# Performance work log

Hardware: AMD Instinct MI355X
Metric: run time of the kernel (lower is better)

## Reference

```python
import jax, jax.numpy as jnp
import numpy as np

B, T, V, E, H = 256, 512, 50000, 300, 128
NORM_GAIN = 0.8     # norm_gain fed at train time
FORGET_BIAS = 1.0
EPS = 1e-12         # tf.contrib.layers.layer_norm default epsilon


def setup_inputs() -> dict:
    key = jax.random.key(0)
    k1, k2, k3 = jax.random.split(key, 3)
    x = jax.random.randint(k1, (B, T), 0, V, dtype=jnp.int32)
    embed = jax.random.normal(k2, (V, E), dtype=jnp.float32)  # tf.random_normal stddev=1
    W = jax.random.normal(k3, (E + H, 4 * H), dtype=jnp.float32) / np.float32(np.sqrt(E + H))
    gains = jnp.full((5, H), NORM_GAIN, dtype=jnp.float32)   # i, j, f, o, cell-transform
    shifts = jnp.zeros((5, H), dtype=jnp.float32)
    return {"x": x, "embed": embed, "W": W, "gains": gains, "shifts": shifts}


def _ln(v, g, b):
    # layer norm over feature axis with learned gain/shift
    m = jnp.mean(v, axis=-1, keepdims=True)
    var = jnp.mean(jnp.square(v - m), axis=-1, keepdims=True)
    return (v - m) * jax.lax.rsqrt(var + EPS) * g + b


def reference(x, embed, W, gains, shifts):
    # embedding: einsum('abc,cd->abd', one_hot(x), embed) == embed[x]
    xe = jnp.take(embed, x, axis=0)            # [B, T, E]
    xe = jnp.transpose(xe, (1, 0, 2))          # [T, B, E] for scan
    c0 = jnp.zeros((x.shape[0], H), jnp.float32)
    h0 = c0

    def step(carry, x_t):
        c, h = carry
        z = jnp.concatenate([x_t, h], axis=-1) @ W      # [B, 4H], no bias
        i, j, f, o = jnp.split(z, 4, axis=-1)
        i = _ln(i, gains[0], shifts[0])
        j = _ln(j, gains[1], shifts[1])
        f = _ln(f, gains[2], shifts[2])
        o = _ln(o, gains[3], shifts[3])
        g = jax.nn.relu(j)                              # activation=tf.nn.relu
        new_c = c * jax.nn.sigmoid(f + FORGET_BIAS) + jax.nn.sigmoid(i) * g
        new_h = jax.nn.relu(_ln(new_c, gains[4], shifts[4])) * jax.nn.sigmoid(o)
        return (new_c, new_h), new_h

    _, ys = jax.lax.scan(step, (c0, h0), xe)            # ys: [T, B, H]
    return jnp.transpose(ys, (1, 0, 2))                 # [B, T, H]
```

## Files before the change

### kernel.cpp

```cpp
#include <hip/hip_runtime.h>
#include <math.h>

#define Bb   256
#define Tt   512
#define Vv   50000
#define Ee   300
#define Hh   128
#define G4   512
#define EPS  1e-12f
#define FBIAS 1.0f
#define RPB  4
#define NBLK (Bb / RPB)

typedef _Float16 half8 __attribute__((ext_vector_type(8)));
typedef float    f32x4 __attribute__((ext_vector_type(4)));

struct F2 { float x, y; };
__device__ inline void fma2(F2& a, const F2 b, const float s) {
    a.x = fmaf(b.x, s, a.x);
    a.y = fmaf(b.y, s, a.y);
}

__global__ __launch_bounds__(256) void embed_proj_kernel(
    const float* __restrict__ embed,
    const float* __restrict__ W,
    float* __restrict__ P)
{
    __shared__ __align__(16) float a[Ee * 32];
    const int r0 = blockIdx.x * 32;
    const int t  = threadIdx.x;

    for (int i = t; i < 32 * Ee; i += 256) {
        int r = i / Ee;
        int k = i - r * Ee;
        int row = r0 + r;
        a[k * 32 + r] = (row < Vv) ? embed[(size_t)row * Ee + k] : 0.0f;
    }
    __syncthreads();

    F2 acc[32];
    #pragma unroll
    for (int r = 0; r < 32; ++r) { acc[r].x = 0.f; acc[r].y = 0.f; }

    const float* wcol = W + 2 * t;
    for (int k = 0; k < Ee; ++k) {
        F2 bv = *(const F2*)(wcol + (size_t)k * G4);
        const float* ak = &a[k * 32];
        #pragma unroll
        for (int r4 = 0; r4 < 32; r4 += 4) {
            float4 av = *(const float4*)(ak + r4);
            fma2(acc[r4 + 0], bv, av.x);
            fma2(acc[r4 + 1], bv, av.y);
            fma2(acc[r4 + 2], bv, av.z);
            fma2(acc[r4 + 3], bv, av.w);
        }
    }

    #pragma unroll
    for (int r = 0; r < 32; ++r) {
        int row = r0 + r;
        if (row < Vv) {
            *(F2*)&P[(size_t)row * G4 + 2 * t] = acc[r];
        }
    }
}

template <int CTRL>
__device__ inline float dpp_mov(float v) {
    return __int_as_float(
        __builtin_amdgcn_update_dpp(0, __float_as_int(v), CTRL, 0xF, 0xF, true));
}
__device__ inline float red16(float v) {
    v += dpp_mov<0xB1>(v);
    v += dpp_mov<0x4E>(v);
    v += dpp_mov<0x141>(v);
    v += dpp_mov<0x140>(v);
    return v;
}
__device__ inline float red64(float v, int bp_addr) {
    v = red16(v);
    v += __int_as_float(__builtin_amdgcn_ds_swizzle(__float_as_int(v), 0x401F));
    v += __int_as_float(__builtin_amdgcn_ds_bpermute(bp_addr, __float_as_int(v)));
    return v;
}

__device__ inline void lds_barrier() {
    __builtin_amdgcn_sched_barrier(0);
    asm volatile("s_waitcnt lgkmcnt(0)" ::: "memory");
    __builtin_amdgcn_sched_barrier(0);
    __builtin_amdgcn_s_barrier();
    __builtin_amdgcn_sched_barrier(0);
}

__device__ inline float sigm(float v) {
    return __fdividef(1.0f, 1.0f + __expf(-v));
}

__global__ __launch_bounds__(256, 1) void lstm_mfma_kernel(
    const float* __restrict__ P,
    const float* __restrict__ W,
    const int*   __restrict__ x,
    const float* __restrict__ gains,
    const float* __restrict__ shifts,
    float* __restrict__ out)
{
    __shared__ __align__(16) float    z_lds[RPB][G4];
    __shared__ __align__(16) float    zn[4][4][Hh];
    __shared__ __align__(16) _Float16 h_lds[16][Hh];

    const int tid  = threadIdx.x;
    const int wv   = tid >> 6;
    const int lane = tid & 63;
    const int bb   = blockIdx.x;

    const int gq   = lane >> 4;
    const int p16  = lane & 15;
    const int col8 = lane * 8;
    const int bp_addr = ((lane ^ 32) << 2);

    {
        uint* hz = (uint*)h_lds;
        #pragma unroll
        for (int i = 0; i < 4; ++i) hz[tid + 256 * i] = 0u;
    }

    half8 bfrag[8][4];
    {
        const int bcol = wv * 128 + p16;
        const int kro  = gq * 8;
        #pragma unroll
        for (int tt = 0; tt < 8; ++tt) {
            #pragma unroll
            for (int ks = 0; ks < 4; ++ks) {
                half8 h;
                #pragma unroll
                for (int j = 0; j < 8; ++j) {
                    h[j] = (_Float16)W[(size_t)(Ee + ks * 32 + kro + j) * G4 + bcol + tt * 16];
                }
                bfrag[tt][ks] = h;
            }
        }
    }

    const float4 g_a = *(const float4*)&gains[col8];
    const float4 g_b = *(const float4*)&gains[col8 + 4];
    const float4 s_a = *(const float4*)&shifts[col8];
    const float4 s_b = *(const float4*)&shifts[col8 + 4];
    const float2 gcell = *(const float2*)&gains[4 * Hh + 2 * lane];
    const float2 scell = *(const float2*)&shifts[4 * Hh + 2 * lane];

    const int row_g = bb * RPB + wv;
    const int* xrow = x + (size_t)row_g * Tt;

    float c0 = 0.f, c1 = 0.f;

    int tok = xrow[0];
    float4 pc0 = *(const float4*)&P[(size_t)tok * G4 + col8];
    float4 pc1 = *(const float4*)&P[(size_t)tok * G4 + col8 + 4];

    char* const hb = (char*)h_lds;
    const int arow = p16;
    const int asw  = (arow & 7) << 4;
    const int kc16 = gq << 4;

    __syncthreads();

    for (int t = 0; t < Tt; ++t) {
        int tn = (t + 1 < Tt) ? t + 1 : Tt - 1;
        int tokn = xrow[tn];
        float4 pn0 = *(const float4*)&P[(size_t)tokn * G4 + col8];
        float4 pn1 = *(const float4*)&P[(size_t)tokn * G4 + col8 + 4];

        half8 af[4];
        #pragma unroll
        for (int ks = 0; ks < 4; ++ks) {
            af[ks] = *(const half8*)(hb + arow * 256 + ((ks * 64 + kc16) ^ asw));
        }

        f32x4 acc[8];
        #pragma unroll
        for (int tt = 0; tt < 8; ++tt) acc[tt] = (f32x4){0.f, 0.f, 0.f, 0.f};
        #pragma unroll
        for (int tt = 0; tt < 8; ++tt) {
            #pragma unroll
            for (int ks = 0; ks < 4; ++ks) {
                acc[tt] = __builtin_amdgcn_mfma_f32_16x16x32_f16(
                    af[ks], bfrag[tt][ks], acc[tt], 0, 0, 0);
            }
        }

        if (lane < 16) {
            #pragma unroll
            for (int tt = 0; tt < 8; ++tt) {
                const int col = wv * 128 + tt * 16 + lane;
                #pragma unroll
                for (int r = 0; r < 4; ++r) z_lds[r][col] = acc[tt][r];
            }
        }

        lds_barrier();

        float zv[8];
        {
            float4 za = *(const float4*)&z_lds[wv][col8];
            float4 zb = *(const float4*)&z_lds[wv][col8 + 4];
            zv[0] = za.x + pc0.x; zv[1] = za.y + pc0.y;
            zv[2] = za.z + pc0.z; zv[3] = za.w + pc0.w;
            zv[4] = zb.x + pc1.x; zv[5] = zb.y + pc1.y;
            zv[6] = zb.z + pc1.z; zv[7] = zb.w + pc1.w;
        }

        float s = 0.f, q = 0.f;
        #pragma unroll
        for (int j = 0; j < 8; ++j) { s += zv[j]; q = fmaf(zv[j], zv[j], q); }
        s = red16(s); q = red16(q);
        {
            const float mean = s * (1.0f / Hh);
            const float var  = q * (1.0f / Hh) - mean * mean;
            const float rstd = rsqrtf(var + EPS);
            const float ga[8] = {g_a.x, g_a.y, g_a.z, g_a.w, g_b.x, g_b.y, g_b.z, g_b.w};
            const float sa[8] = {s_a.x, s_a.y, s_a.z, s_a.w, s_b.x, s_b.y, s_b.z, s_b.w};
            #pragma unroll
            for (int j = 0; j < 8; ++j)
                zv[j] = (zv[j] - mean) * rstd * ga[j] + sa[j];
        }

        *(float4*)&zn[wv][gq][p16 * 8]     = (float4){zv[0], zv[1], zv[2], zv[3]};
        *(float4*)&zn[wv][gq][p16 * 8 + 4] = (float4){zv[4], zv[5], zv[6], zv[7]};

        float2 iv = *(const float2*)&zn[wv][0][2 * lane];
        float2 jv = *(const float2*)&zn[wv][1][2 * lane];
        float2 fv = *(const float2*)&zn[wv][2][2 * lane];
        float2 ov = *(const float2*)&zn[wv][3][2 * lane];

        c0 = c0 * sigm(fv.x + FBIAS) + sigm(iv.x) * fmaxf(jv.x, 0.f);
        c1 = c1 * sigm(fv.y + FBIAS) + sigm(iv.y) * fmaxf(jv.y, 0.f);

        float s2 = c0 + c1;
        float q2 = fmaf(c0, c0, c1 * c1);
        s2 = red64(s2, bp_addr); q2 = red64(q2, bp_addr);
        const float m2 = s2 * (1.0f / Hh);
        const float v2 = q2 * (1.0f / Hh) - m2 * m2;
        const float r2 = rsqrtf(v2 + EPS);
        const float lc0 = (c0 - m2) * r2 * gcell.x + scell.x;
        const float lc1 = (c1 - m2) * r2 * gcell.y + scell.y;
        const float h0 = fmaxf(lc0, 0.f) * sigm(ov.x);
        const float h1 = fmaxf(lc1, 0.f) * sigm(ov.y);

        {
            union { _Float16 hh[2]; uint u; } pk;
            pk.hh[0] = (_Float16)h0; pk.hh[1] = (_Float16)h1;
            *(uint*)(hb + wv * 256 + ((4 * lane) ^ (wv << 4))) = pk.u;
        }
        *(float2*)&out[((size_t)row_g * Tt + t) * Hh + 2 * lane] = (float2){h0, h1};

        lds_barrier();

        pc0 = pn0; pc1 = pn1;
    }
}

extern "C" void kernel_launch(void* const* d_in, const int* in_sizes, int n_in,
                              void* d_out, int out_size, void* d_ws, size_t ws_size,
                              hipStream_t stream) {
    const int*   x      = (const int*)d_in[0];
    const float* embed  = (const float*)d_in[1];
    const float* W      = (const float*)d_in[2];
    const float* gains  = (const float*)d_in[3];
    const float* shifts = (const float*)d_in[4];
    float* out = (float*)d_out;

    float* P = (float*)d_ws;

    embed_proj_kernel<<<dim3((Vv + 31) / 32), dim3(256), 0, stream>>>(embed, W, P);
    lstm_mfma_kernel<<<dim3(NBLK), dim3(256), 0, stream>>>(P, W, x, gains, shifts, out);
}
```

Before: 903.2 us.

## Use MFMA for embedding projection and ping-pong two LSTM teams per block

The fp32 FMA embedding-projection kernel is replaced by a persistent f16 MFMA kernel that converts embed rows into swizzled LDS tiles. The LSTM kernel now runs 512 threads as two 4-wave teams, each handling two batch rows. The teams alternate the MFMA recurrent matmul and the layernorm/cell phase, so matrix and vector work from different rows can overlap while only half the waves do elementwise work. The 64-lane reduction also moves from swizzle/bpermute to DPP row broadcasts plus readlane, and fp16 embed inputs slightly change precision.

New measurement: 1.062 ms. 17.6% more time.

```diff
diff --git a/kernel.cpp b/kernel.cpp
--- a/kernel.cpp
+++ b/kernel.cpp
@@ -9,61 +9,9 @@
 #define G4   512
 #define EPS  1e-12f
 #define FBIAS 1.0f
-#define RPB  4
-#define NBLK (Bb / RPB)
 
 typedef _Float16 half8 __attribute__((ext_vector_type(8)));
 typedef float    f32x4 __attribute__((ext_vector_type(4)));
-
-struct F2 { float x, y; };
-__device__ inline void fma2(F2& a, const F2 b, const float s) {
-    a.x = fmaf(b.x, s, a.x);
-    a.y = fmaf(b.y, s, a.y);
-}
-
-__global__ __launch_bounds__(256) void embed_proj_kernel(
-    const float* __restrict__ embed,
-    const float* __restrict__ W,
-    float* __restrict__ P)
-{
-    __shared__ __align__(16) float a[Ee * 32];
-    const int r0 = blockIdx.x * 32;
-    const int t  = threadIdx.x;
-
-    for (int i = t; i < 32 * Ee; i += 256) {
-        int r = i / Ee;
-        int k = i - r * Ee;
-        int row = r0 + r;
-        a[k * 32 + r] = (row < Vv) ? embed[(size_t)row * Ee + k] : 0.0f;
-    }
-    __syncthreads();
-
-    F2 acc[32];
-    #pragma unroll
-    for (int r = 0; r < 32; ++r) { acc[r].x = 0.f; acc[r].y = 0.f; }
-
-    const float* wcol = W + 2 * t;
-    for (int k = 0; k < Ee; ++k) {
-        F2 bv = *(const F2*)(wcol + (size_t)k * G4);
-        const float* ak = &a[k * 32];
-        #pragma unroll
-        for (int r4 = 0; r4 < 32; r4 += 4) {
-            float4 av = *(const float4*)(ak + r4);
-            fma2(acc[r4 + 0], bv, av.x);
-            fma2(acc[r4 + 1], bv, av.y);
-            fma2(acc[r4 + 2], bv, av.z);
-            fma2(acc[r4 + 3], bv, av.w);
-        }
-    }
-
-    #pragma unroll
-    for (int r = 0; r < 32; ++r) {
-        int row = r0 + r;
-        if (row < Vv) {
-            *(F2*)&P[(size_t)row * G4 + 2 * t] = acc[r];
-        }
-    }
-}
 
 template <int CTRL>
 __device__ inline float dpp_mov(float v) {
@@ -77,11 +25,11 @@
     v += dpp_mov<0x140>(v);
     return v;
 }
-__device__ inline float red64(float v, int bp_addr) {
+__device__ inline float red64b(float v) {
     v = red16(v);
-    v += __int_as_float(__builtin_amdgcn_ds_swizzle(__float_as_int(v), 0x401F));
-    v += __int_as_float(__builtin_amdgcn_ds_bpermute(bp_addr, __float_as_int(v)));
-    return v;
+    v += dpp_mov<0x142>(v);
+    v += dpp_mov<0x143>(v);
+    return __int_as_float(__builtin_amdgcn_readlane(__float_as_int(v), 63));
 }
 
 __device__ inline void lds_barrier() {
@@ -96,7 +44,99 @@
     return __fdividef(1.0f, 1.0f + __expf(-v));
 }
 
-__global__ __launch_bounds__(256, 1) void lstm_mfma_kernel(
+#define PROJ_TILES ((Vv + 31) / 32)
+
+__global__ __launch_bounds__(512, 2) void embed_proj_mfma(
+    const float* __restrict__ embed,
+    const float* __restrict__ W,
+    float* __restrict__ P)
+{
+    __shared__ __align__(16) _Float16 A[32 * 320];
+
+    const int tid  = threadIdx.x;
+    const int wv   = tid >> 6;
+    const int lane = tid & 63;
+    const int p16  = lane & 15;
+    const int gq   = lane >> 4;
+
+    half8 bf[4][10];
+    #pragma unroll
+    for (int tt = 0; tt < 4; ++tt) {
+        #pragma unroll
+        for (int ks = 0; ks < 10; ++ks) {
+            half8 h;
+            #pragma unroll
+            for (int j = 0; j < 8; ++j) {
+                int k = ks * 32 + gq * 8 + j;
+                h[j] = (k < Ee)
+                     ? (_Float16)W[(size_t)k * G4 + wv * 64 + tt * 16 + p16]
+                     : (_Float16)0.f;
+            }
+            bf[tt][ks] = h;
+        }
+    }
+
+    char* const Ab = (char*)A;
+    for (int i = tid; i < 32 * 10; i += 512) {
+        int row = i / 10, m = i - row * 10;
+        *(uint*)(Ab + ((row * 640 + 600 + m * 4) ^ ((row & 7) << 4))) = 0u;
+    }
+    __syncthreads();
+
+    for (int mtile = blockIdx.x; mtile < PROJ_TILES; mtile += gridDim.x) {
+        const int r0 = mtile * 32;
+
+        for (int i = tid; i < 32 * 75; i += 512) {
+            int row = i / 75, k4 = i - row * 75;
+            int grow = r0 + row;
+            float4 v = (grow < Vv) ? *(const float4*)&embed[(size_t)grow * Ee + k4 * 4]
+                                   : (float4){0.f, 0.f, 0.f, 0.f};
+            union { _Float16 h[4]; uint2 u; } pk;
+            pk.h[0] = (_Float16)v.x; pk.h[1] = (_Float16)v.y;
+            pk.h[2] = (_Float16)v.z; pk.h[3] = (_Float16)v.w;
+            *(uint2*)(Ab + ((row * 640 + k4 * 8) ^ ((row & 7) << 4))) = pk.u;
+        }
+        __syncthreads();
+
+        f32x4 acc[2][4];
+        #pragma unroll
+        for (int mt = 0; mt < 2; ++mt)
+            #pragma unroll
+            for (int tt = 0; tt < 4; ++tt)
+                acc[mt][tt] = (f32x4){0.f, 0.f, 0.f, 0.f};
+
+        #pragma unroll
+        for (int mt = 0; mt < 2; ++mt) {
+            const int arow = mt * 16 + p16;
+            #pragma unroll
+            for (int ks = 0; ks < 10; ++ks) {
+                half8 af = *(const half8*)(Ab + ((arow * 640 + ks * 64 + gq * 16)
+                                                 ^ ((arow & 7) << 4)));
+                #pragma unroll
+                for (int tt = 0; tt < 4; ++tt)
+                    acc[mt][tt] = __builtin_amdgcn_mfma_f32_16x16x32_f16(
+                        af, bf[tt][ks], acc[mt][tt], 0, 0, 0);
+            }
+        }
+
+        #pragma unroll
+        for (int mt = 0; mt < 2; ++mt)
+            #pragma unroll
+            for (int tt = 0; tt < 4; ++tt)
+                #pragma unroll
+                for (int r = 0; r < 4; ++r) {
+                    int row = r0 + mt * 16 + gq * 4 + r;
+                    if (row < Vv)
+                        P[(size_t)row * G4 + wv * 64 + tt * 16 + p16] = acc[mt][tt][r];
+                }
+        __syncthreads();
+    }
+}
+
+#define TROWS 2
+#define LBLK  (Bb / (2 * TROWS))
+
+__global__ __launch_bounds__(512, 2) void lstm_mfma2(
     const float* __restrict__ P,
     const float* __restrict__ W,
     const int*   __restrict__ x,
@@ -104,41 +144,38 @@
     const float* __restrict__ shifts,
     float* __restrict__ out)
 {
-    __shared__ __align__(16) float    z_lds[RPB][G4];
-    __shared__ __align__(16) float    zn[4][4][Hh];
-    __shared__ __align__(16) _Float16 h_lds[16][Hh];
+    __shared__ __align__(16) float    z_all[2][2048];
+    __shared__ __align__(16) float    zn_all[4][4][Hh];
+    __shared__ __align__(16) _Float16 h_all[2][16][Hh];
 
     const int tid  = threadIdx.x;
-    const int wv   = tid >> 6;
+    const int wv8  = tid >> 6;
+    const int team = wv8 >> 2;
+    const int twv  = wv8 & 3;
     const int lane = tid & 63;
-    const int bb   = blockIdx.x;
-
     const int gq   = lane >> 4;
     const int p16  = lane & 15;
     const int col8 = lane * 8;
-    const int bp_addr = ((lane ^ 32) << 2);
+    const int bb   = blockIdx.x;
 
     {
-        uint* hz = (uint*)h_lds;
-        #pragma unroll
-        for (int i = 0; i < 4; ++i) hz[tid + 256 * i] = 0u;
+        uint* hz = (uint*)h_all;
+        #pragma unroll
+        for (int i = 0; i < 4; ++i) hz[tid + 512 * i] = 0u;
     }
 
     half8 bfrag[8][4];
-    {
-        const int bcol = wv * 128 + p16;
-        const int kro  = gq * 8;
-        #pragma unroll
-        for (int tt = 0; tt < 8; ++tt) {
-            #pragma unroll
-            for (int ks = 0; ks < 4; ++ks) {
-                half8 h;
-                #pragma unroll
-                for (int j = 0; j < 8; ++j) {
-                    h[j] = (_Float16)W[(size_t)(Ee + ks * 32 + kro + j) * G4 + bcol + tt * 16];
-                }
-                bfrag[tt][ks] = h;
-            }
+    #pragma unroll
+    for (int tt = 0; tt < 8; ++tt) {
+        #pragma unroll
+        for (int ks = 0; ks < 4; ++ks) {
+            half8 h;
+            #pragma unroll
+            for (int j = 0; j < 8; ++j) {
+                h[j] = (_Float16)W[(size_t)(Ee + ks * 32 + gq * 8 + j) * G4
+                                   + twv * 128 + tt * 16 + p16];
+            }
+            bfrag[tt][ks] = h;
         }
     }
 
@@ -149,114 +186,125 @@
     const float2 gcell = *(const float2*)&gains[4 * Hh + 2 * lane];
     const float2 scell = *(const float2*)&shifts[4 * Hh + 2 * lane];
 
-    const int row_g = bb * RPB + wv;
-    const int* xrow = x + (size_t)row_g * Tt;
+    const bool lnw   = (twv < TROWS);
+    const int  lrow  = twv;
+    const int  row_g = bb * (2 * TROWS) + team * TROWS + twv;
+    const int* xrow  = x + (size_t)row_g * Tt;
 
     float c0 = 0.f, c1 = 0.f;
-
-    int tok = xrow[0];
-    float4 pc0 = *(const float4*)&P[(size_t)tok * G4 + col8];
-    float4 pc1 = *(const float4*)&P[(size_t)tok * G4 + col8 + 4];
-
-    char* const hb = (char*)h_lds;
-    const int arow = p16;
-    const int asw  = (arow & 7) << 4;
-    const int kc16 = gq << 4;
+    float4 pc0 = {0,0,0,0}, pc1 = {0,0,0,0};
+    int tokr = lnw ? xrow[0] : 0;
+
+    char*  const hb  = (char*)&h_all[team][0][0];
+    float* const zt  = &z_all[team][0];
+    float* const znt = &zn_all[team * 2 + (lnw ? twv : 0)][0][0];
 
     __syncthreads();
 
-    for (int t = 0; t < Tt; ++t) {
-        int tn = (t + 1 < Tt) ? t + 1 : Tt - 1;
-        int tokn = xrow[tn];
-        float4 pn0 = *(const float4*)&P[(size_t)tokn * G4 + col8];
-        float4 pn1 = *(const float4*)&P[(size_t)tokn * G4 + col8 + 4];
-
-        half8 af[4];
-        #pragma unroll
-        for (int ks = 0; ks < 4; ++ks) {
-            af[ks] = *(const half8*)(hb + arow * 256 + ((ks * 64 + kc16) ^ asw));
-        }
-
-        f32x4 acc[8];
-        #pragma unroll
-        for (int tt = 0; tt < 8; ++tt) acc[tt] = (f32x4){0.f, 0.f, 0.f, 0.f};
-        #pragma unroll
-        for (int tt = 0; tt < 8; ++tt) {
+    for (int i = 0; i <= 2 * Tt; ++i) {
+        const int  ms   = i >> 1;
+        const bool do_m = ((i & 1) == team) && (ms < Tt);
+        const int  ls   = (i - 1) >> 1;
+        const bool do_l = ((i & 1) != team) && (i >= 1) && (ls < Tt);
+
+        if (do_m) {
+            if (lnw) {
+                pc0 = *(const float4*)&P[(size_t)tokr * G4 + col8];
+                pc1 = *(const float4*)&P[(size_t)tokr * G4 + col8 + 4];
+                int nst = (ms + 1 < Tt) ? ms + 1 : Tt - 1;
+                tokr = xrow[nst];
+            }
+
+            half8 af[4];
             #pragma unroll
             for (int ks = 0; ks < 4; ++ks) {
-                acc[tt] = __builtin_amdgcn_mfma_f32_16x16x32_f16(
-                    af[ks], bfrag[tt][ks], acc[tt], 0, 0, 0);
-            }
-        }
-
-        if (lane < 16) {
+                af[ks] = *(const half8*)(hb + p16 * 256
+                              + ((ks * 64 + (gq << 4)) ^ ((p16 & 7) << 4)));
+            }
+
+            f32x4 acc[8];
+            #pragma unroll
+            for (int tt = 0; tt < 8; ++tt) acc[tt] = (f32x4){0.f, 0.f, 0.f, 0.f};
             #pragma unroll
             for (int tt = 0; tt < 8; ++tt) {
-                const int col = wv * 128 + tt * 16 + lane;
-                #pragma unroll
-                for (int r = 0; r < 4; ++r) z_lds[r][col] = acc[tt][r];
-            }
-        }
-
-        lds_barrier();
-
-        float zv[8];
-        {
-            float4 za = *(const float4*)&z_lds[wv][col8];
-            float4 zb = *(const float4*)&z_lds[wv][col8 + 4];
+                #pragma unroll
+                for (int ks = 0; ks < 4; ++ks) {
+                    acc[tt] = __builtin_amdgcn_mfma_f32_16x16x32_f16(
+                        af[ks], bfrag[tt][ks], acc[tt], 0, 0, 0);
+                }
+            }
+
+            if (lane < 16) {
+                #pragma unroll
+                for (int tt = 0; tt < 8; ++tt) {
+                    const int cb = twv * 8 + tt;
+                    float* zp = zt + cb * 64 + (p16 ^ ((cb & 3) << 2));
+                    #pragma unroll
+                    for (int r = 0; r < 4; ++r) zp[r * 16] = acc[tt][r];
+                }
+            }
+        }
+
+        if (do_l && lnw) {
+            const int cb0  = lane >> 1;
+            const int wb   = 8 * (lane & 1);
+            const int mxor = (cb0 & 3) << 2;
+            const int b1   = wb ^ mxor;
+            const float* zp = zt + cb0 * 64 + lrow * 16;
+            float4 za = *(const float4*)(zp + b1);
+            float4 zb = *(const float4*)(zp + (b1 ^ 4));
+
+            float zv[8];
             zv[0] = za.x + pc0.x; zv[1] = za.y + pc0.y;
             zv[2] = za.z + pc0.z; zv[3] = za.w + pc0.w;
             zv[4] = zb.x + pc1.x; zv[5] = zb.y + pc1.y;
             zv[6] = zb.z + pc1.z; zv[7] = zb.w + pc1.w;
-        }
-
-        float s = 0.f, q = 0.f;
-        #pragma unroll
-        for (int j = 0; j < 8; ++j) { s += zv[j]; q = fmaf(zv[j], zv[j], q); }
-        s = red16(s); q = red16(q);
-        {
-            const float mean = s * (1.0f / Hh);
-            const float var  = q * (1.0f / Hh) - mean * mean;
-            const float rstd = rsqrtf(var + EPS);
-            const float ga[8] = {g_a.x, g_a.y, g_a.z, g_a.w, g_b.x, g_b.y, g_b.z, g_b.w};
-            const float sa[8] = {s_a.x, s_a.y, s_a.z, s_a.w, s_b.x, s_b.y, s_b.z, s_b.w};
-            #pragma unroll
-            for (int j = 0; j < 8; ++j)
-                zv[j] = (zv[j] - mean) * rstd * ga[j] + sa[j];
-        }
-
-        *(float4*)&zn[wv][gq][p16 * 8]     = (float4){zv[0], zv[1], zv[2], zv[3]};
-        *(float4*)&zn[wv][gq][p16 * 8 + 4] = (float4){zv[4], zv[5], zv[6], zv[7]};
-
-        float2 iv = *(const float2*)&zn[wv][0][2 * lane];
-        float2 jv = *(const float2*)&zn[wv][1][2 * lane];
-        float2 fv = *(const float2*)&zn[wv][2][2 * lane];
-        float2 ov = *(const float2*)&zn[wv][3][2 * lane];
-
-        c0 = c0 * sigm(fv.x + FBIAS) + sigm(iv.x) * fmaxf(jv.x, 0.f);
-        c1 = c1 * sigm(fv.y + FBIAS) + sigm(iv.y) * fmaxf(jv.y, 0.f);
-
-        float s2 = c0 + c1;
-        float q2 = fmaf(c0, c0, c1 * c1);
-        s2 = red64(s2, bp_addr); q2 = red64(q2, bp_addr);
-        const float m2 = s2 * (1.0f / Hh);
-        const float v2 = q2 * (1.0f / Hh) - m2 * m2;
-        const float r2 = rsqrtf(v2 + EPS);
-        const float lc0 = (c0 - m2) * r2 * gcell.x + scell.x;
-        const float lc1 = (c1 - m2) * r2 * gcell.y + scell.y;
-        const float h0 = fmaxf(lc0, 0.f) * sigm(ov.x);
-        const float h1 = fmaxf(lc1, 0.f) * sigm(ov.y);
-
-        {
-            union { _Float16 hh[2]; uint u; } pk;
-            pk.hh[0] = (_Float16)h0; pk.hh[1] = (_Float16)h1;
-            *(uint*)(hb + wv * 256 + ((4 * lane) ^ (wv << 4))) = pk.u;
-        }
-        *(float2*)&out[((size_t)row_g * Tt + t) * Hh + 2 * lane] = (float2){h0, h1};
+
+            float s = 0.f, q = 0.f;
+            #pragma unroll
+            for (int j = 0; j < 8; ++j) { s += zv[j]; q = fmaf(zv[j], zv[j], q); }
+            s = red16(s); q = red16(q);
+            {
+                const float mean = s * (1.0f / Hh);
+                const float var  = q * (1.0f / Hh) - mean * mean;
+                const float rstd = rsqrtf(var + EPS);
+                const float ga[8] = {g_a.x, g_a.y, g_a.z, g_a.w, g_b.x, g_b.y, g_b.z, g_b.w};
+                const float sa[8] = {s_a.x, s_a.y, s_a.z, s_a.w, s_b.x, s_b.y, s_b.z, s_b.w};
+                #pragma unroll
+                for (int j = 0; j < 8; ++j)
+                    zv[j] = (zv[j] - mean) * rstd * ga[j] + sa[j];
+            }
+
+            *(float4*)&znt[gq * Hh + p16 * 8]     = (float4){zv[0], zv[1], zv[2], zv[3]};
+            *(float4*)&znt[gq * Hh + p16 * 8 + 4] = (float4){zv[4], zv[5], zv[6], zv[7]};
+
+            float2 iv = *(const float2*)&znt[0 * Hh + 2 * lane];
+            float2 jv = *(const float2*)&znt[1 * Hh + 2 * lane];
+            float2 fv = *(const float2*)&znt[2 * Hh + 2 * lane];
+            float2 ov = *(const float2*)&znt[3 * Hh + 2 * lane];
+
+            c0 = c0 * sigm(fv.x + FBIAS) + sigm(iv.x) * fmaxf(jv.x, 0.f);
+            c1 = c1 * sigm(fv.y + FBIAS) + sigm(iv.y) * fmaxf(jv.y, 0.f);
+
+            float s2 = red64b(c0 + c1);
+            float q2 = red64b(fmaf(c0, c0, c1 * c1));
+            const float m2 = s2 * (1.0f / Hh);
+            const float v2 = q2 * (1.0f / Hh) - m2 * m2;
+            const float r2 = rsqrtf(v2 + EPS);
+            const float lc0 = (c0 - m2) * r2 * gcell.x + scell.x;
+            const float lc1 = (c1 - m2) * r2 * gcell.y + scell.y;
+            const float h0 = fmaxf(lc0, 0.f) * sigm(ov.x);
+            const float h1 = fmaxf(lc1, 0.f) * sigm(ov.y);
+
+            {
+                union { _Float16 hh[2]; uint u; } pk;
+                pk.hh[0] = (_Float16)h0; pk.hh[1] = (_Float16)h1;
+                *(uint*)(hb + lrow * 256 + ((4 * lane) ^ (lrow << 4))) = pk.u;
+            }
+            *(float2*)&out[((size_t)row_g * Tt + ls) * Hh + 2 * lane] = (float2){h0, h1};
+        }
 
         lds_barrier();
-
-        pc0 = pn0; pc1 = pn1;
     }
 }
 
@@ -272,6 +320,6 @@
 
     float* P = (float*)d_ws;
 
-    embed_proj_kernel<<<dim3((Vv + 31) / 32), dim3(256), 0, stream>>>(embed, W, P);
-    lstm_mfma_kernel<<<dim3(NBLK), dim3(256), 0, stream>>>(P, W, x, gains, shifts, out);
-}
+    embed_proj_mfma<<<dim3(256), dim3(512), 0, stream>>>(embed, W, P);
+    lstm_mfma2<<<dim3(LBLK), dim3(512), 0, stream>>>(P, W, x, gains, shifts, out);
+}
```
